# Optimization experiments

Measured on AMD Instinct MI355X. Metric: run time of the kernel, lower is better.

The kernel has to match this reference:

```python
import jax, jax.numpy as jnp
import numpy as np

C = 1.0          # ball curvature (k = -1/c with c=1.0 in the torch module)
SQC = 1.0        # sqrt(C)
LN_EPS = 1e-5

def _artanh(x):
    return jnp.arctanh(jnp.clip(x, -1.0 + 1e-7, 1.0 - 1e-7))

def _norm(x):
    # last-dim L2 norm, clamped away from zero for stable division
    return jnp.clip(jnp.sqrt(jnp.sum(x * x, axis=-1, keepdims=True)), 1e-7, None)

def expmap0(u):
    un = _norm(u)
    return jnp.tanh(SQC * un) * u / (SQC * un)

def logmap0(y):
    yn = _norm(y)
    return _artanh(SQC * yn) * y / (SQC * yn)

def mobius_add(x, y):
    x2 = jnp.sum(x * x, axis=-1, keepdims=True)
    y2 = jnp.sum(y * y, axis=-1, keepdims=True)
    xy = jnp.sum(x * y, axis=-1, keepdims=True)
    num = (1.0 + 2.0 * C * xy + C * y2) * x + (1.0 - C * x2) * y
    den = 1.0 + 2.0 * C * xy + C * C * x2 * y2
    return num / jnp.clip(den, 1e-15, None)

def mobius_matvec(W, x):
    # W: [H, D], x: [B, D] -> [B, H]
    mx = x @ W.T
    xn = _norm(x)
    mxn = _norm(mx)
    res = jnp.tanh(mxn / xn * _artanh(SQC * xn)) * mx / (SQC * mxn)
    return jnp.where(mxn <= 1e-7, jnp.zeros_like(res), res)

def mobius_pointwise_mul(w, x):
    wx = w * x
    xn = _norm(x)
    wxn = _norm(wx)
    res = jnp.tanh(wxn / xn * _artanh(SQC * xn)) * wx / (SQC * wxn)
    return jnp.where(wxn <= 1e-7, jnp.zeros_like(res), res)

def layer_norm(x, g, b):
    mu = jnp.mean(x, axis=-1, keepdims=True)
    var = jnp.mean((x - mu) ** 2, axis=-1, keepdims=True)
    return (x - mu) * jax.lax.rsqrt(var + LN_EPS) * g + b

def one_rnn_transform(W, h, U, x, b):
    Wh = mobius_matvec(W, h)
    Ux = mobius_matvec(U, x)
    return mobius_add(mobius_add(Wh, Ux), b)

def setup_inputs() -> dict:
    key = jax.random.key(0)
    B, I, H = 65536, 256, 256
    k1, k2, k3, k4, k5 = jax.random.split(key, 5)
    stdv = 1.0 / np.sqrt(H)
    # points on the Poincare ball via expmap0 of small tangent vectors
    x = expmap0(0.02 * jax.random.normal(k1, (B, I), dtype=jnp.float32))
    hx = expmap0(0.02 * jax.random.normal(k2, (B, H), dtype=jnp.float32))
    weight_ih = jax.random.uniform(k3, (3 * H, I), dtype=jnp.float32, minval=-stdv, maxval=stdv)
    weight_hh = jax.random.uniform(k4, (3 * H, H), dtype=jnp.float32, minval=-stdv, maxval=stdv)
    bias = 0.01 * jax.random.normal(k5, (3, H), dtype=jnp.float32)
    ln_gamma = jnp.ones((3, H), dtype=jnp.float32)
    ln_beta = jnp.zeros((3, H), dtype=jnp.float32)
    return {"input": x, "hx": hx, "weight_ih": weight_ih, "weight_hh": weight_hh,
            "bias": bias, "ln_gamma": ln_gamma, "ln_beta": ln_beta}

def reference(input, hx, weight_ih, weight_hh, bias, ln_gamma, ln_beta):
    H = hx.shape[-1]
    W_ir, W_ih_, W_iz = weight_ih[:H], weight_ih[H:2*H], weight_ih[2*H:]
    W_hr, W_hh_, W_hz = weight_hh[:H], weight_hh[H:2*H], weight_hh[2*H:]
    b_r, b_h, b_z = bias[0], bias[1], bias[2]
    temp_z = logmap0(one_rnn_transform(W_hz, hx, W_iz, input, b_z))
    temp_r = logmap0(one_rnn_transform(W_hr, hx, W_ir, input, b_r))
    z_t = jax.nn.sigmoid(layer_norm(temp_z, ln_gamma[0], ln_beta[0]))
    r_t = jax.nn.sigmoid(layer_norm(temp_r, ln_gamma[1], ln_beta[1]))
    rh_t = mobius_pointwise_mul(r_t, hx)
    h_tilde = one_rnn_transform(W_hh_, rh_t, W_ih_, input, b_h)
    h_tilde = expmap0(jnp.tanh(layer_norm(logmap0(h_tilde), ln_gamma[2], ln_beta[2])))
    temp_1 = mobius_pointwise_mul(1.0 - z_t, hx)
    temp_2 = mobius_pointwise_mul(z_t, h_tilde)
    return mobius_add(temp_1, temp_2)
```

## Files before the change

kernel.cpp:

```cpp
#include <hip/hip_runtime.h>
#include <math.h>

#define HD  256
#define BM  16
#define NTH 256

typedef __attribute__((ext_vector_type(8))) short bf16x8;
typedef __attribute__((ext_vector_type(4))) float f32x4;

__device__ __forceinline__ float rcp_f(float x){ return __builtin_amdgcn_rcpf(x); }
__device__ __forceinline__ float tanh_f(float x){
  float ax = fabsf(x);
  float e  = __expf(-2.f*ax);
  float t  = (1.f - e) * rcp_f(1.f + e);
  return copysignf(t, x);
}
__device__ __forceinline__ float artanh_f(float v){
  v = fminf(fmaxf(v, -1.f + 1e-7f), 1.f - 1e-7f);
  return 0.5f * __logf((1.f + v) * rcp_f(1.f - v));
}
__device__ __forceinline__ float sigmoid_f(float v){ return rcp_f(1.f + __expf(-v)); }
__device__ __forceinline__ unsigned short f2bf(float f){
  unsigned u = __float_as_uint(f);
  u += 0x7FFFu + ((u >> 16) & 1u);
  return (unsigned short)(u >> 16);
}
__device__ __forceinline__ float bf2f(unsigned short h){
  return __uint_as_float(((unsigned)h) << 16);
}
__device__ __forceinline__ int swz(int R, int C){
  return R*HD + (((C >> 3) ^ (R & 7)) << 3) + (C & 7);
}

__global__ void convert_w_kernel(const float* __restrict__ Wih,
                                 const float* __restrict__ Whh,
                                 unsigned short* __restrict__ wb){
  int c = blockIdx.x * blockDim.x + threadIdx.x;
  if (c >= 6 * 8192) return;
  int mat = c >> 13;
  int ci  = c & 8191;
  int l = ci & 63, st = ci >> 6;
  int s = st & 7, ct = st >> 3;
  int col = ct * 16 + (l & 15);
  int k0  = s * 32 + (l >> 4) * 8;
  const float* src = (mat < 3) ? (Wih + (size_t)mat * HD * HD)
                               : (Whh + (size_t)(mat - 3) * HD * HD);
  const float* p = src + (size_t)col * HD + k0;
  unsigned short tmp[8];
  #pragma unroll
  for (int j = 0; j < 8; ++j) tmp[j] = f2bf(p[j]);
  *(bf16x8*)(wb + (size_t)mat * 65536 + (size_t)ci * 8) = *(bf16x8*)tmp;
}

__device__ __forceinline__ void gate_gemm(
    const unsigned short* ldsH, const unsigned short* __restrict__ wH,
    const unsigned short* ldsX, const unsigned short* __restrict__ wX,
    f32x4 A[4], f32x4 Bx[4], int wc, int lr, int lg, int l){
  #pragma unroll
  for (int n = 0; n < 4; ++n){
    A[n]  = (f32x4){0.f,0.f,0.f,0.f};
    Bx[n] = (f32x4){0.f,0.f,0.f,0.f};
  }
  #pragma unroll
  for (int s = 0; s < 8; ++s){
    int idx = lr*HD + (((4*s + lg) ^ (lr & 7)) << 3);
    bf16x8 ah = *(const bf16x8*)&ldsH[idx];
    bf16x8 ax = *(const bf16x8*)&ldsX[idx];
    #pragma unroll
    for (int n = 0; n < 4; ++n){
      int ct = wc*4 + n;
      int off = ((ct*8 + s)*64 + l)*8;
      bf16x8 bh = *(const bf16x8*)(wH + off);
      bf16x8 bx = *(const bf16x8*)(wX + off);
      A[n]  = __builtin_amdgcn_mfma_f32_16x16x32_bf16(ah, bh, A[n], 0, 0, 0);
      Bx[n] = __builtin_amdgcn_mfma_f32_16x16x32_bf16(ax, bx, Bx[n], 0, 0, 0);
    }
  }
}

__device__ __forceinline__ void gate_reduce_chain(
    const f32x4 (&A)[4], const f32x4 (&Bx)[4], const float (&bt)[4],
    float (*RED)[33], float (*kco)[9], float (*srow)[BM], const float* sbb,
    int rowA, int gidx, int t, int wc, int lr, int lg){
  float p[7][4];
  #pragma unroll
  for (int q = 0; q < 4; ++q){
    float a2=0.f,b2=0.f,ab=0.f,sA=0.f,sB=0.f,Ab=0.f,Bb=0.f;
    #pragma unroll
    for (int n = 0; n < 4; ++n){
      float ae = A[n][q], be = Bx[n][q], bv = bt[n];
      a2 = fmaf(ae,ae,a2); b2 = fmaf(be,be,b2); ab = fmaf(ae,be,ab);
      sA += ae; sB += be; Ab = fmaf(ae,bv,Ab); Bb = fmaf(be,bv,Bb);
    }
    p[0][q]=a2; p[1][q]=b2; p[2][q]=ab; p[3][q]=sA; p[4][q]=sB; p[5][q]=Ab; p[6][q]=Bb;
  }
  #pragma unroll
  for (int j = 0; j < 7; ++j)
    #pragma unroll
    for (int q = 0; q < 4; ++q){
      float v = p[j][q];
      v += __shfl_xor(v,1); v += __shfl_xor(v,2);
      v += __shfl_xor(v,4); v += __shfl_xor(v,8);
      p[j][q] = v;
    }
  if (lr == 0){
    #pragma unroll
    for (int q = 0; q < 4; ++q){
      int R = lg*4 + q;
      #pragma unroll
      for (int j = 0; j < 7; ++j) RED[R][wc*8 + j] = p[j][q];
    }
  }
  __syncthreads();
  if (t < BM){
    int R = t;
    float s[7];
    #pragma unroll
    for (int j = 0; j < 7; ++j)
      s[j] = RED[R][j] + RED[R][8+j] + RED[R][16+j] + RED[R][24+j];
    float bb  = sbb[gidx];
    float sbs = sbb[4+gidx];
    float an = srow[rowA][R], aa = srow[rowA+1][R];
    float bn = srow[0][R],    ba = srow[1][R];
    float mraw = sqrtf(s[0]); float mA = fmaxf(mraw, 1e-7f);
    float tA = tanh_f(mA / an * aa);
    float sa  = (mraw <= 1e-7f) ? 0.f : tA / mA;
    float x2a = (mraw <= 1e-7f) ? 0.f : tA*tA;
    float nraw = sqrtf(s[1]); float mB = fmaxf(nraw, 1e-7f);
    float tB = tanh_f(mB / bn * ba);
    float sb_ = (nraw <= 1e-7f) ? 0.f : tB / mB;
    float x2b = (nraw <= 1e-7f) ? 0.f : tB*tB;
    float xy = sa*sb_*s[2];
    float ca = 1.f + 2.f*xy + x2b;
    float cb = 1.f - x2a;
    float den = fmaxf(1.f + 2.f*xy + x2a*x2b, 1e-15f);
    float u = ca*sa/den, v = cb*sb_/den;
    float P2 = u*u*s[0] + 2.f*u*v*s[2] + v*v*s[1];
    float Pb = u*s[5] + v*s[6];
    float sP = u*s[3] + v*s[4];
    float ca2 = 1.f + 2.f*Pb + bb;
    float cb2 = 1.f - P2;
    float den2 = fmaxf(1.f + 2.f*Pb + P2*bb, 1e-15f);
    float pp = ca2/den2, ww = cb2/den2;
    float Q2 = pp*pp*P2 + 2.f*pp*ww*Pb + ww*ww*bb;
    float sQsum = pp*sP + ww*sbs;
    float qn = fmaxf(sqrtf(Q2), 1e-7f);
    float sQ = artanh_f(qn) / qn;
    float mu = sQ*sQsum*(1.f/HD);
    float e2 = sQ*sQ*Q2*(1.f/HD);
    float is = rsqrtf(e2 - mu*mu + 1e-5f);
    kco[R][0] = sQ*pp*u;  kco[R][1] = sQ*pp*v;  kco[R][2] = sQ*ww;
    kco[R][3] = mu;       kco[R][4] = is;
  }
  __syncthreads();
}

__global__ __launch_bounds__(NTH, 2) void mobius_gru_mfma(
    const float* __restrict__ x, const float* __restrict__ hx,
    const unsigned short* __restrict__ wbih, const unsigned short* __restrict__ wbhh,
    const float* __restrict__ bias, const float* __restrict__ gam,
    const float* __restrict__ bet, float* __restrict__ out, int B){
  __shared__ unsigned short xb[BM*HD];
  __shared__ unsigned short hb[BM*HD];
  __shared__ float RED[BM][33];
  __shared__ float kco[BM][9];
  __shared__ float srow[8][BM];
  __shared__ float sbb[8];

  const int t  = threadIdx.x;
  const int l  = t & 63;
  const int lr = l & 15, lg = l >> 4;
  const int wc = t >> 6;
  const size_t row0 = (size_t)blockIdx.x * BM;

  {
    float* spart = &RED[0][0];
    int r = t >> 4, seg = t & 15;
    const float* xp = x  + (row0 + r)*HD + seg*16;
    const float* hp = hx + (row0 + r)*HD + seg*16;
    float sx = 0.f, sh = 0.f;
    #pragma unroll
    for (int i = 0; i < 4; ++i){
      int c = seg*16 + i*4;
      int di = swz(r, c);
      float4 v = *(const float4*)(xp + i*4);
      sx += v.x*v.x + v.y*v.y + v.z*v.z + v.w*v.w;
      ushort4 o = { f2bf(v.x), f2bf(v.y), f2bf(v.z), f2bf(v.w) };
      *(ushort4*)&xb[di] = o;
      v = *(const float4*)(hp + i*4);
      sh += v.x*v.x + v.y*v.y + v.z*v.z + v.w*v.w;
      ushort4 o2 = { f2bf(v.x), f2bf(v.y), f2bf(v.z), f2bf(v.w) };
      *(ushort4*)&hb[di] = o2;
    }
    spart[r*16 + seg] = sx; spart[256 + r*16 + seg] = sh;
  }
  if (t >= 64 && t < 256){
    int g = (t >> 6) - 1;
    float4 b4 = *(const float4*)&bias[g*HD + (t & 63)*4];
    float p2 = b4.x*b4.x + b4.y*b4.y + b4.z*b4.z + b4.w*b4.w;
    float ps = b4.x + b4.y + b4.z + b4.w;
    #pragma unroll
    for (int m = 1; m <= 32; m <<= 1){ p2 += __shfl_xor(p2, m); ps += __shfl_xor(ps, m); }
    if ((t & 63) == 0){ sbb[g] = p2; sbb[4+g] = ps; }
  }
  __syncthreads();
  if (t < BM){
    float* spart = &RED[0][0];
    float sx = 0.f, sh = 0.f;
    #pragma unroll
    for (int i = 0; i < 16; ++i){ sx += spart[t*16 + i]; sh += spart[256 + t*16 + i]; }
    float xn = fmaxf(sqrtf(sx), 1e-7f);
    float hn = fmaxf(sqrtf(sh), 1e-7f);
    srow[0][t] = xn; srow[1][t] = artanh_f(xn);
    srow[2][t] = hn; srow[3][t] = artanh_f(hn);
  }
  __syncthreads();

  f32x4 A[4], Bx[4];
  float bt[4], gv[4], bv[4];
  unsigned ztp[4][2];
  float hvreg[4][4];

  #pragma unroll
  for (int n = 0; n < 4; ++n){
    int C = wc*64 + n*16 + lr;
    bt[n] = bias[2*HD + C]; gv[n] = gam[C]; bv[n] = bet[C];
  }
  gate_gemm(hb, wbhh + 2*65536, xb, wbih + 2*65536, A, Bx, wc, lr, lg, l);
  gate_reduce_chain(A, Bx, bt, RED, kco, srow, sbb, 2, 2, t, wc, lr, lg);
  #pragma unroll
  for (int q = 0; q < 4; ++q){
    int R = lg*4 + q;
    float KA=kco[R][0], KB=kco[R][1], Kb=kco[R][2], mu=kco[R][3], is=kco[R][4];
    #pragma unroll
    for (int n = 0; n < 4; ++n){
      float ln = (KA*A[n][q] + KB*Bx[n][q] + Kb*bt[n] - mu)*is*gv[n] + bv[n];
      unsigned zb = f2bf(sigmoid_f(ln));
      if ((q & 1) == 0) ztp[n][q>>1] = zb;
      else              ztp[n][q>>1] |= (zb << 16);
    }
  }

  #pragma unroll
  for (int n = 0; n < 4; ++n){
    int C = wc*64 + n*16 + lr;
    bt[n] = bias[C]; gv[n] = gam[HD + C]; bv[n] = bet[HD + C];
  }
  gate_gemm(hb, wbhh, xb, wbih, A, Bx, wc, lr, lg, l);
  gate_reduce_chain(A, Bx, bt, RED, kco, srow, sbb, 2, 0, t, wc, lr, lg);
  {
    #pragma unroll
    for (int q = 0; q < 4; ++q){
      int R = lg*4 + q;
      float KA=kco[R][0], KB=kco[R][1], Kb=kco[R][2], mu=kco[R][3], is=kco[R][4];
      float acc = 0.f;
      #pragma unroll
      for (int n = 0; n < 4; ++n){
        int C = wc*64 + n*16 + lr;
        float hv = bf2f(hb[swz(R, C)]);
        hvreg[n][q] = hv;
        float ln = (KA*A[n][q] + KB*Bx[n][q] + Kb*bt[n] - mu)*is*gv[n] + bv[n];
        float rhv = sigmoid_f(ln) * hv;
        Bx[n][q] = rhv;
        acc = fmaf(rhv, rhv, acc);
      }
      float v2 = acc;
      v2 += __shfl_xor(v2,1); v2 += __shfl_xor(v2,2);
      v2 += __shfl_xor(v2,4); v2 += __shfl_xor(v2,8);
      if (lr == 0) RED[R][wc*8] = v2;
    }
  }
  __syncthreads();
  if (t < BM){
    int R = t;
    float s0 = RED[R][0] + RED[R][8] + RED[R][16] + RED[R][24];
    float wraw = sqrtf(s0); float wn = fmaxf(wraw, 1e-7f);
    float s = tanh_f(wn / srow[2][R] * srow[3][R]);
    float sc = (wraw <= 1e-7f) ? 0.f : s / wn;
    float rn = fmaxf((wraw <= 1e-7f) ? 0.f : fabsf(s), 1e-7f);
    kco[R][0] = sc; srow[4][R] = rn; srow[5][R] = artanh_f(rn);
  }
  __syncthreads();
  #pragma unroll
  for (int q = 0; q < 4; ++q){
    int R = lg*4 + q;
    float sc = kco[R][0];
    #pragma unroll
    for (int n = 0; n < 4; ++n){
      int C = wc*64 + n*16 + lr;
      hb[swz(R, C)] = f2bf(sc * Bx[n][q]);
    }
  }
  __syncthreads();

  #pragma unroll
  for (int n = 0; n < 4; ++n){
    int C = wc*64 + n*16 + lr;
    bt[n] = bias[HD + C]; gv[n] = gam[2*HD + C]; bv[n] = bet[2*HD + C];
  }
  gate_gemm(hb, wbhh + 65536, xb, wbih + 65536, A, Bx, wc, lr, lg, l);
  gate_reduce_chain(A, Bx, bt, RED, kco, srow, sbb, 4, 1, t, wc, lr, lg);
  {
    #pragma unroll
    for (int q = 0; q < 4; ++q){
      int R = lg*4 + q;
      float KA=kco[R][0], KB=kco[R][1], Kb=kco[R][2], mu=kco[R][3], is=kco[R][4];
      float acc = 0.f;
      #pragma unroll
      for (int n = 0; n < 4; ++n){
        float ln = (KA*A[n][q] + KB*Bx[n][q] + Kb*bt[n] - mu)*is*gv[n] + bv[n];
        float uv = tanh_f(ln);
        A[n][q] = uv;
        acc = fmaf(uv, uv, acc);
      }
      float v2 = acc;
      v2 += __shfl_xor(v2,1); v2 += __shfl_xor(v2,2);
      v2 += __shfl_xor(v2,4); v2 += __shfl_xor(v2,8);
      if (lr == 0) RED[R][wc*8] = v2;
    }
  }
  __syncthreads();
  if (t < BM){
    int R = t;
    float s0 = RED[R][0] + RED[R][8] + RED[R][16] + RED[R][24];
    float unraw = sqrtf(s0);
    float un = fmaxf(unraw, 1e-7f);
    float es = tanh_f(un) / un;
    float htn = fmaxf(es * unraw, 1e-7f);
    kco[R][0] = es; srow[6][R] = htn; srow[7][R] = artanh_f(htn);
  }
  __syncthreads();

  #pragma unroll
  for (int q = 0; q < 4; ++q){
    int R = lg*4 + q;
    float es = kco[R][0];
    float a1 = 0.f, a2 = 0.f, a12 = 0.f;
    #pragma unroll
    for (int n = 0; n < 4; ++n){
      unsigned zp = ztp[n][q >> 1];
      float zv = __uint_as_float((q & 1) ? (zp & 0xFFFF0000u) : (zp << 16));
      float w2v = zv * es * A[n][q];
      float w1v = (1.f - zv) * hvreg[n][q];
      A[n][q]  = w1v;
      Bx[n][q] = w2v;
      a1 = fmaf(w1v, w1v, a1); a2 = fmaf(w2v, w2v, a2); a12 = fmaf(w1v, w2v, a12);
    }
    float v1 = a1, v2 = a2, v3 = a12;
    v1 += __shfl_xor(v1,1); v2 += __shfl_xor(v2,1); v3 += __shfl_xor(v3,1);
    v1 += __shfl_xor(v1,2); v2 += __shfl_xor(v2,2); v3 += __shfl_xor(v3,2);
    v1 += __shfl_xor(v1,4); v2 += __shfl_xor(v2,4); v3 += __shfl_xor(v3,4);
    v1 += __shfl_xor(v1,8); v2 += __shfl_xor(v2,8); v3 += __shfl_xor(v3,8);
    if (lr == 0){
      RED[R][wc*8]   = v1;
      RED[R][wc*8+1] = v2;
      RED[R][wc*8+2] = v3;
    }
  }
  __syncthreads();
  if (t < BM){
    int R = t;
    float s1  = RED[R][0] + RED[R][8]  + RED[R][16] + RED[R][24];
    float s2  = RED[R][1] + RED[R][9]  + RED[R][17] + RED[R][25];
    float s12 = RED[R][2] + RED[R][10] + RED[R][18] + RED[R][26];
    float raw1 = sqrtf(s1); float n1 = fmaxf(raw1, 1e-7f);
    float ss1 = tanh_f(n1 / srow[2][R] * srow[3][R]);
    float sc1 = (raw1 <= 1e-7f) ? 0.f : ss1 / n1;
    float t1  = (raw1 <= 1e-7f) ? 0.f : ss1*ss1;
    float raw2 = sqrtf(s2); float n2 = fmaxf(raw2, 1e-7f);
    float ss2 = tanh_f(n2 / srow[6][R] * srow[7][R]);
    float sc2 = (raw2 <= 1e-7f) ? 0.f : ss2 / n2;
    float t2  = (raw2 <= 1e-7f) ? 0.f : ss2*ss2;
    float xy = sc1*sc2*s12;
    float ca = 1.f + 2.f*xy + t2;
    float cb = 1.f - t1;
    float den = fmaxf(1.f + 2.f*xy + t1*t2, 1e-15f);
    kco[R][0] = ca*sc1/den;
    kco[R][1] = cb*sc2/den;
  }
  __syncthreads();
  #pragma unroll
  for (int q = 0; q < 4; ++q){
    int R = lg*4 + q;
    float cw1 = kco[R][0], cw2 = kco[R][1];
    #pragma unroll
    for (int n = 0; n < 4; ++n){
      int C = wc*64 + n*16 + lr;
      out[(row0 + R)*HD + C] = cw1*A[n][q] + cw2*Bx[n][q];
    }
  }
}

extern "C" void kernel_launch(void* const* d_in, const int* in_sizes, int n_in,
                              void* d_out, int out_size, void* d_ws, size_t ws_size,
                              hipStream_t stream){
  const float* x    = (const float*)d_in[0];
  const float* hx   = (const float*)d_in[1];
  const float* Wih  = (const float*)d_in[2];
  const float* Whh  = (const float*)d_in[3];
  const float* bias = (const float*)d_in[4];
  const float* gam  = (const float*)d_in[5];
  const float* bet  = (const float*)d_in[6];
  float* out = (float*)d_out;
  unsigned short* wb = (unsigned short*)d_ws;
  const int B = in_sizes[0] / HD;

  hipLaunchKernelGGL(convert_w_kernel, dim3(192), dim3(256), 0, stream, Wih, Whh, wb);
  hipLaunchKernelGGL(mobius_gru_mfma, dim3(B / BM), dim3(NTH), 0, stream,
                     x, hx, wb, wb + 3*65536, bias, gam, bet, out, B);
}
```

Before: 222.8 us.

## Fuse z, r and x-side h-gate GEMMs into one pass with shared reductions

Merges the z-gate and r-gate GEMMs, plus the input-side GEMM of the candidate gate, into a single k-loop that reuses the LDS A-fragments for five MFMA streams. The z and r per-row reduction chains now run together in 32 threads with separate reduction buffers, which removes several barrier rounds. Register pressure rises a lot (five accumulator sets of 4 f32x4 each live at once), which could cause spills or lower occupancy under the 2-block launch bound.

```diff
diff --git a/kernel.cpp b/kernel.cpp
--- a/kernel.cpp
+++ b/kernel.cpp
@@ -52,43 +52,16 @@
   *(bf16x8*)(wb + (size_t)mat * 65536 + (size_t)ci * 8) = *(bf16x8*)tmp;
 }
 
-__device__ __forceinline__ void gate_gemm(
-    const unsigned short* ldsH, const unsigned short* __restrict__ wH,
-    const unsigned short* ldsX, const unsigned short* __restrict__ wX,
-    f32x4 A[4], f32x4 Bx[4], int wc, int lr, int lg, int l){
-  #pragma unroll
-  for (int n = 0; n < 4; ++n){
-    A[n]  = (f32x4){0.f,0.f,0.f,0.f};
-    Bx[n] = (f32x4){0.f,0.f,0.f,0.f};
-  }
-  #pragma unroll
-  for (int s = 0; s < 8; ++s){
-    int idx = lr*HD + (((4*s + lg) ^ (lr & 7)) << 3);
-    bf16x8 ah = *(const bf16x8*)&ldsH[idx];
-    bf16x8 ax = *(const bf16x8*)&ldsX[idx];
-    #pragma unroll
-    for (int n = 0; n < 4; ++n){
-      int ct = wc*4 + n;
-      int off = ((ct*8 + s)*64 + l)*8;
-      bf16x8 bh = *(const bf16x8*)(wH + off);
-      bf16x8 bx = *(const bf16x8*)(wX + off);
-      A[n]  = __builtin_amdgcn_mfma_f32_16x16x32_bf16(ah, bh, A[n], 0, 0, 0);
-      Bx[n] = __builtin_amdgcn_mfma_f32_16x16x32_bf16(ax, bx, Bx[n], 0, 0, 0);
-    }
-  }
-}
-
-__device__ __forceinline__ void gate_reduce_chain(
-    const f32x4 (&A)[4], const f32x4 (&Bx)[4], const float (&bt)[4],
-    float (*RED)[33], float (*kco)[9], float (*srow)[BM], const float* sbb,
-    int rowA, int gidx, int t, int wc, int lr, int lg){
+__device__ __forceinline__ void reduce7(
+    const f32x4* A, const f32x4* B, const float* bt,
+    float (*RED)[33], int wc, int lr, int lg){
   float p[7][4];
   #pragma unroll
   for (int q = 0; q < 4; ++q){
     float a2=0.f,b2=0.f,ab=0.f,sA=0.f,sB=0.f,Ab=0.f,Bb=0.f;
     #pragma unroll
     for (int n = 0; n < 4; ++n){
-      float ae = A[n][q], be = Bx[n][q], bv = bt[n];
+      float ae = A[n][q], be = B[n][q], bv = bt[n];
       a2 = fmaf(ae,ae,a2); b2 = fmaf(be,be,b2); ab = fmaf(ae,be,ab);
       sA += ae; sB += be; Ab = fmaf(ae,bv,Ab); Bb = fmaf(be,bv,Bb);
     }
@@ -111,48 +84,40 @@
       for (int j = 0; j < 7; ++j) RED[R][wc*8 + j] = p[j][q];
     }
   }
-  __syncthreads();
-  if (t < BM){
-    int R = t;
-    float s[7];
-    #pragma unroll
-    for (int j = 0; j < 7; ++j)
-      s[j] = RED[R][j] + RED[R][8+j] + RED[R][16+j] + RED[R][24+j];
-    float bb  = sbb[gidx];
-    float sbs = sbb[4+gidx];
-    float an = srow[rowA][R], aa = srow[rowA+1][R];
-    float bn = srow[0][R],    ba = srow[1][R];
-    float mraw = sqrtf(s[0]); float mA = fmaxf(mraw, 1e-7f);
-    float tA = tanh_f(mA / an * aa);
-    float sa  = (mraw <= 1e-7f) ? 0.f : tA / mA;
-    float x2a = (mraw <= 1e-7f) ? 0.f : tA*tA;
-    float nraw = sqrtf(s[1]); float mB = fmaxf(nraw, 1e-7f);
-    float tB = tanh_f(mB / bn * ba);
-    float sb_ = (nraw <= 1e-7f) ? 0.f : tB / mB;
-    float x2b = (nraw <= 1e-7f) ? 0.f : tB*tB;
-    float xy = sa*sb_*s[2];
-    float ca = 1.f + 2.f*xy + x2b;
-    float cb = 1.f - x2a;
-    float den = fmaxf(1.f + 2.f*xy + x2a*x2b, 1e-15f);
-    float u = ca*sa/den, v = cb*sb_/den;
-    float P2 = u*u*s[0] + 2.f*u*v*s[2] + v*v*s[1];
-    float Pb = u*s[5] + v*s[6];
-    float sP = u*s[3] + v*s[4];
-    float ca2 = 1.f + 2.f*Pb + bb;
-    float cb2 = 1.f - P2;
-    float den2 = fmaxf(1.f + 2.f*Pb + P2*bb, 1e-15f);
-    float pp = ca2/den2, ww = cb2/den2;
-    float Q2 = pp*pp*P2 + 2.f*pp*ww*Pb + ww*ww*bb;
-    float sQsum = pp*sP + ww*sbs;
-    float qn = fmaxf(sqrtf(Q2), 1e-7f);
-    float sQ = artanh_f(qn) / qn;
-    float mu = sQ*sQsum*(1.f/HD);
-    float e2 = sQ*sQ*Q2*(1.f/HD);
-    float is = rsqrtf(e2 - mu*mu + 1e-5f);
-    kco[R][0] = sQ*pp*u;  kco[R][1] = sQ*pp*v;  kco[R][2] = sQ*ww;
-    kco[R][3] = mu;       kco[R][4] = is;
-  }
-  __syncthreads();
+}
+
+__device__ __forceinline__ void chain5(
+    const float* s, float bb, float sbs,
+    float an, float aa, float bn, float ba, float* o){
+  float mraw = sqrtf(s[0]); float mA = fmaxf(mraw, 1e-7f);
+  float tA = tanh_f(mA / an * aa);
+  float sa  = (mraw <= 1e-7f) ? 0.f : tA / mA;
+  float x2a = (mraw <= 1e-7f) ? 0.f : tA*tA;
+  float nraw = sqrtf(s[1]); float mB = fmaxf(nraw, 1e-7f);
+  float tB = tanh_f(mB / bn * ba);
+  float sb_ = (nraw <= 1e-7f) ? 0.f : tB / mB;
+  float x2b = (nraw <= 1e-7f) ? 0.f : tB*tB;
+  float xy = sa*sb_*s[2];
+  float ca = 1.f + 2.f*xy + x2b;
+  float cb = 1.f - x2a;
+  float den = fmaxf(1.f + 2.f*xy + x2a*x2b, 1e-15f);
+  float u = ca*sa/den, v = cb*sb_/den;
+  float P2 = u*u*s[0] + 2.f*u*v*s[2] + v*v*s[1];
+  float Pb = u*s[5] + v*s[6];
+  float sP = u*s[3] + v*s[4];
+  float ca2 = 1.f + 2.f*Pb + bb;
+  float cb2 = 1.f - P2;
+  float den2 = fmaxf(1.f + 2.f*Pb + P2*bb, 1e-15f);
+  float pp = ca2/den2, ww = cb2/den2;
+  float Q2 = pp*pp*P2 + 2.f*pp*ww*Pb + ww*ww*bb;
+  float sQsum = pp*sP + ww*sbs;
+  float qn = fmaxf(sqrtf(Q2), 1e-7f);
+  float sQ = artanh_f(qn) / qn;
+  float mu = sQ*sQsum*(1.f/HD);
+  float e2 = sQ*sQ*Q2*(1.f/HD);
+  float is = rsqrtf(e2 - mu*mu + 1e-5f);
+  o[0] = sQ*pp*u;  o[1] = sQ*pp*v;  o[2] = sQ*ww;
+  o[3] = mu;       o[4] = is;
 }
 
 __global__ __launch_bounds__(NTH, 2) void mobius_gru_mfma(
@@ -162,8 +127,9 @@
     const float* __restrict__ bet, float* __restrict__ out, int B){
   __shared__ unsigned short xb[BM*HD];
   __shared__ unsigned short hb[BM*HD];
-  __shared__ float RED[BM][33];
-  __shared__ float kco[BM][9];
+  __shared__ float REDZ[BM][33];
+  __shared__ float REDR[BM][33];
+  __shared__ float kco[BM][10];
   __shared__ float srow[8][BM];
   __shared__ float sbb[8];
 
@@ -174,7 +140,7 @@
   const size_t row0 = (size_t)blockIdx.x * BM;
 
   {
-    float* spart = &RED[0][0];
+    float* spart = &REDZ[0][0];
     int r = t >> 4, seg = t & 15;
     const float* xp = x  + (row0 + r)*HD + seg*16;
     const float* hp = hx + (row0 + r)*HD + seg*16;
@@ -205,7 +171,7 @@
   }
   __syncthreads();
   if (t < BM){
-    float* spart = &RED[0][0];
+    float* spart = &REDZ[0][0];
     float sx = 0.f, sh = 0.f;
     #pragma unroll
     for (int i = 0; i < 16; ++i){ sx += spart[t*16 + i]; sh += spart[256 + t*16 + i]; }
@@ -216,39 +182,166 @@
   }
   __syncthreads();
 
-  f32x4 A[4], Bx[4];
-  float bt[4], gv[4], bv[4];
+  f32x4 Az[4], Bz[4], Ar[4], Br[4], Bh[4];
+  float btz[4], btr[4];
+  #pragma unroll
+  for (int n = 0; n < 4; ++n){
+    int C = wc*64 + n*16 + lr;
+    btz[n] = bias[2*HD + C];
+    btr[n] = bias[C];
+    Az[n] = (f32x4){0.f,0.f,0.f,0.f}; Bz[n] = (f32x4){0.f,0.f,0.f,0.f};
+    Ar[n] = (f32x4){0.f,0.f,0.f,0.f}; Br[n] = (f32x4){0.f,0.f,0.f,0.f};
+    Bh[n] = (f32x4){0.f,0.f,0.f,0.f};
+  }
+  {
+    const unsigned short* wHz = wbhh + 2*65536;
+    const unsigned short* wXz = wbih + 2*65536;
+    const unsigned short* wHr = wbhh;
+    const unsigned short* wXr = wbih;
+    const unsigned short* wXh = wbih + 65536;
+    #pragma unroll
+    for (int s = 0; s < 8; ++s){
+      int idx = lr*HD + (((4*s + lg) ^ (lr & 7)) << 3);
+      bf16x8 ah = *(const bf16x8*)&hb[idx];
+      bf16x8 ax = *(const bf16x8*)&xb[idx];
+      #pragma unroll
+      for (int n = 0; n < 4; ++n){
+        int off = (((wc*4 + n)*8 + s)*64 + l)*8;
+        bf16x8 bhz = *(const bf16x8*)(wHz + off);
+        bf16x8 bxz = *(const bf16x8*)(wXz + off);
+        bf16x8 bhr = *(const bf16x8*)(wHr + off);
+        bf16x8 bxr = *(const bf16x8*)(wXr + off);
+        bf16x8 bxh = *(const bf16x8*)(wXh + off);
+        Az[n] = __builtin_amdgcn_mfma_f32_16x16x32_bf16(ah, bhz, Az[n], 0, 0, 0);
+        Bz[n] = __builtin_amdgcn_mfma_f32_16x16x32_bf16(ax, bxz, Bz[n], 0, 0, 0);
+        Ar[n] = __builtin_amdgcn_mfma_f32_16x16x32_bf16(ah, bhr, Ar[n], 0, 0, 0);
+        Br[n] = __builtin_amdgcn_mfma_f32_16x16x32_bf16(ax, bxr, Br[n], 0, 0, 0);
+        Bh[n] = __builtin_amdgcn_mfma_f32_16x16x32_bf16(ax, bxh, Bh[n], 0, 0, 0);
+      }
+    }
+  }
+  reduce7(Az, Bz, btz, REDZ, wc, lr, lg);
+  reduce7(Ar, Br, btr, REDR, wc, lr, lg);
+  __syncthreads();
+  if (t < 32){
+    int R = t & 15, gsel = t >> 4;
+    float (*REDp)[33] = gsel ? REDR : REDZ;
+    int gidx = gsel ? 0 : 2;
+    float s[7];
+    #pragma unroll
+    for (int j = 0; j < 7; ++j)
+      s[j] = REDp[R][j] + REDp[R][8+j] + REDp[R][16+j] + REDp[R][24+j];
+    float o[5];
+    chain5(s, sbb[gidx], sbb[4+gidx],
+           srow[2][R], srow[3][R], srow[0][R], srow[1][R], o);
+    #pragma unroll
+    for (int k = 0; k < 5; ++k) kco[R][gsel*5 + k] = o[k];
+  }
+  __syncthreads();
+
   unsigned ztp[4][2];
   float hvreg[4][4];
-
+  {
+    float gvz[4], bvz[4], gvr[4], bvr[4];
+    #pragma unroll
+    for (int n = 0; n < 4; ++n){
+      int C = wc*64 + n*16 + lr;
+      gvz[n] = gam[C];      bvz[n] = bet[C];
+      gvr[n] = gam[HD + C]; bvr[n] = bet[HD + C];
+    }
+    #pragma unroll
+    for (int q = 0; q < 4; ++q){
+      int R = lg*4 + q;
+      float KAz=kco[R][0], KBz=kco[R][1], Kbz=kco[R][2], muz=kco[R][3], isz=kco[R][4];
+      float KAr=kco[R][5], KBr=kco[R][6], Kbr=kco[R][7], mur=kco[R][8], isr=kco[R][9];
+      float acc = 0.f;
+      #pragma unroll
+      for (int n = 0; n < 4; ++n){
+        int C = wc*64 + n*16 + lr;
+        float hv = bf2f(hb[swz(R, C)]);
+        hvreg[n][q] = hv;
+        float lnz = (KAz*Az[n][q] + KBz*Bz[n][q] + Kbz*btz[n] - muz)*isz*gvz[n] + bvz[n];
+        unsigned zb = f2bf(sigmoid_f(lnz));
+        if ((q & 1) == 0) ztp[n][q>>1] = zb;
+        else              ztp[n][q>>1] |= (zb << 16);
+        float lnr = (KAr*Ar[n][q] + KBr*Br[n][q] + Kbr*btr[n] - mur)*isr*gvr[n] + bvr[n];
+        float rhv = sigmoid_f(lnr) * hv;
+        Br[n][q] = rhv;
+        acc = fmaf(rhv, rhv, acc);
+      }
+      float v2 = acc;
+      v2 += __shfl_xor(v2,1); v2 += __shfl_xor(v2,2);
+      v2 += __shfl_xor(v2,4); v2 += __shfl_xor(v2,8);
+      if (lr == 0) REDZ[R][wc*8] = v2;
+    }
+  }
+  __syncthreads();
+  if (t < BM){
+    int R = t;
+    float s0 = REDZ[R][0] + REDZ[R][8] + REDZ[R][16] + REDZ[R][24];
+    float wraw = sqrtf(s0); float wn = fmaxf(wraw, 1e-7f);
+    float s = tanh_f(wn / srow[2][R] * srow[3][R]);
+    float sc = (wraw <= 1e-7f) ? 0.f : s / wn;
+    float rn = fmaxf((wraw <= 1e-7f) ? 0.f : fabsf(s), 1e-7f);
+    kco[R][0] = sc; srow[4][R] = rn; srow[5][R] = artanh_f(rn);
+  }
+  __syncthreads();
+  #pragma unroll
+  for (int q = 0; q < 4; ++q){
+    int R = lg*4 + q;
+    float sc = kco[R][0];
+    #pragma unroll
+    for (int n = 0; n < 4; ++n){
+      int C = wc*64 + n*16 + lr;
+      hb[swz(R, C)] = f2bf(sc * Br[n][q]);
+    }
+  }
+  __syncthreads();
+
+  f32x4 Ah[4];
+  float bth[4];
   #pragma unroll
   for (int n = 0; n < 4; ++n){
     int C = wc*64 + n*16 + lr;
-    bt[n] = bias[2*HD + C]; gv[n] = gam[C]; bv[n] = bet[C];
-  }
-  gate_gemm(hb, wbhh + 2*65536, xb, wbih + 2*65536, A, Bx, wc, lr, lg, l);
-  gate_reduce_chain(A, Bx, bt, RED, kco, srow, sbb, 2, 2, t, wc, lr, lg);
-  #pragma unroll
-  for (int q = 0; q < 4; ++q){
-    int R = lg*4 + q;
-    float KA=kco[R][0], KB=kco[R][1], Kb=kco[R][2], mu=kco[R][3], is=kco[R][4];
-    #pragma unroll
-    for (int n = 0; n < 4; ++n){
-      float ln = (KA*A[n][q] + KB*Bx[n][q] + Kb*bt[n] - mu)*is*gv[n] + bv[n];
-      unsigned zb = f2bf(sigmoid_f(ln));
-      if ((q & 1) == 0) ztp[n][q>>1] = zb;
-      else              ztp[n][q>>1] |= (zb << 16);
-    }
-  }
-
-  #pragma unroll
-  for (int n = 0; n < 4; ++n){
-    int C = wc*64 + n*16 + lr;
-    bt[n] = bias[C]; gv[n] = gam[HD + C]; bv[n] = bet[HD + C];
-  }
-  gate_gemm(hb, wbhh, xb, wbih, A, Bx, wc, lr, lg, l);
-  gate_reduce_chain(A, Bx, bt, RED, kco, srow, sbb, 2, 0, t, wc, lr, lg);
+    bth[n] = bias[HD + C];
+    Ah[n] = (f32x4){0.f,0.f,0.f,0.f};
+  }
   {
+    const unsigned short* wHh = wbhh + 65536;
+    #pragma unroll
+    for (int s = 0; s < 8; ++s){
+      int idx = lr*HD + (((4*s + lg) ^ (lr & 7)) << 3);
+      bf16x8 ar = *(const bf16x8*)&hb[idx];
+      #pragma unroll
+      for (int n = 0; n < 4; ++n){
+        int off = (((wc*4 + n)*8 + s)*64 + l)*8;
+        bf16x8 bh = *(const bf16x8*)(wHh + off);
+        Ah[n] = __builtin_amdgcn_mfma_f32_16x16x32_bf16(ar, bh, Ah[n], 0, 0, 0);
+      }
+    }
+  }
+  reduce7(Ah, Bh, bth, REDZ, wc, lr, lg);
+  __syncthreads();
+  if (t < BM){
+    int R = t;
+    float s[7];
+    #pragma unroll
+    for (int j = 0; j < 7; ++j)
+      s[j] = REDZ[R][j] + REDZ[R][8+j] + REDZ[R][16+j] + REDZ[R][24+j];
+    float o[5];
+    chain5(s, sbb[1], sbb[5],
+           srow[4][R], srow[5][R], srow[0][R], srow[1][R], o);
+    #pragma unroll
+    for (int k = 0; k < 5; ++k) kco[R][k] = o[k];
+  }
+  __syncthreads();
+  {
+    float gvh[4], bvh[4];
+    #pragma unroll
+    for (int n = 0; n < 4; ++n){
+      int C = wc*64 + n*16 + lr;
+      gvh[n] = gam[2*HD + C]; bvh[n] = bet[2*HD + C];
+    }
     #pragma unroll
     for (int q = 0; q < 4; ++q){
       int R = lg*4 + q;
@@ -256,73 +349,21 @@
       float acc = 0.f;
       #pragma unroll
       for (int n = 0; n < 4; ++n){
-        int C = wc*64 + n*16 + lr;
-        float hv = bf2f(hb[swz(R, C)]);
-        hvreg[n][q] = hv;
-        float ln = (KA*A[n][q] + KB*Bx[n][q] + Kb*bt[n] - mu)*is*gv[n] + bv[n];
-        float rhv = sigmoid_f(ln) * hv;
-        Bx[n][q] = rhv;
-        acc = fmaf(rhv, rhv, acc);
-      }
-      float v2 = acc;
-      v2 += __shfl_xor(v2,1); v2 += __shfl_xor(v2,2);
-      v2 += __shfl_xor(v2,4); v2 += __shfl_xor(v2,8);
-      if (lr == 0) RED[R][wc*8] = v2;
-    }
-  }
-  __syncthreads();
-  if (t < BM){
-    int R = t;
-    float s0 = RED[R][0] + RED[R][8] + RED[R][16] + RED[R][24];
-    float wraw = sqrtf(s0); float wn = fmaxf(wraw, 1e-7f);
-    float s = tanh_f(wn / srow[2][R] * srow[3][R]);
-    float sc = (wraw <= 1e-7f) ? 0.f : s / wn;
-    float rn = fmaxf((wraw <= 1e-7f) ? 0.f : fabsf(s), 1e-7f);
-    kco[R][0] = sc; srow[4][R] = rn; srow[5][R] = artanh_f(rn);
-  }
-  __syncthreads();
-  #pragma unroll
-  for (int q = 0; q < 4; ++q){
-    int R = lg*4 + q;
-    float sc = kco[R][0];
-    #pragma unroll
-    for (int n = 0; n < 4; ++n){
-      int C = wc*64 + n*16 + lr;
-      hb[swz(R, C)] = f2bf(sc * Bx[n][q]);
-    }
-  }
-  __syncthreads();
-
-  #pragma unroll
-  for (int n = 0; n < 4; ++n){
-    int C = wc*64 + n*16 + lr;
-    bt[n] = bias[HD + C]; gv[n] = gam[2*HD + C]; bv[n] = bet[2*HD + C];
-  }
-  gate_gemm(hb, wbhh + 65536, xb, wbih + 65536, A, Bx, wc, lr, lg, l);
-  gate_reduce_chain(A, Bx, bt, RED, kco, srow, sbb, 4, 1, t, wc, lr, lg);
-  {
-    #pragma unroll
-    for (int q = 0; q < 4; ++q){
-      int R = lg*4 + q;
-      float KA=kco[R][0], KB=kco[R][1], Kb=kco[R][2], mu=kco[R][3], is=kco[R][4];
-      float acc = 0.f;
-      #pragma unroll
-      for (int n = 0; n < 4; ++n){
-        float ln = (KA*A[n][q] + KB*Bx[n][q] + Kb*bt[n] - mu)*is*gv[n] + bv[n];
+        float ln = (KA*Ah[n][q] + KB*Bh[n][q] + Kb*bth[n] - mu)*is*gvh[n] + bvh[n];
         float uv = tanh_f(ln);
-        A[n][q] = uv;
+        Ah[n][q] = uv;
         acc = fmaf(uv, uv, acc);
       }
       float v2 = acc;
       v2 += __shfl_xor(v2,1); v2 += __shfl_xor(v2,2);
       v2 += __shfl_xor(v2,4); v2 += __shfl_xor(v2,8);
-      if (lr == 0) RED[R][wc*8] = v2;
+      if (lr == 0) REDZ[R][wc*8] = v2;
     }
   }
   __syncthreads();
   if (t < BM){
     int R = t;
-    float s0 = RED[R][0] + RED[R][8] + RED[R][16] + RED[R][24];
+    float s0 = REDZ[R][0] + REDZ[R][8] + REDZ[R][16] + REDZ[R][24];
     float unraw = sqrtf(s0);
     float un = fmaxf(unraw, 1e-7f);
     float es = tanh_f(un) / un;
@@ -340,10 +381,10 @@
     for (int n = 0; n < 4; ++n){
       unsigned zp = ztp[n][q >> 1];
       float zv = __uint_as_float((q & 1) ? (zp & 0xFFFF0000u) : (zp << 16));
-      float w2v = zv * es * A[n][q];
+      float w2v = zv * es * Ah[n][q];
       float w1v = (1.f - zv) * hvreg[n][q];
-      A[n][q]  = w1v;
-      Bx[n][q] = w2v;
+      Ah[n][q] = w2v;
+      Bh[n][q] = w1v;
       a1 = fmaf(w1v, w1v, a1); a2 = fmaf(w2v, w2v, a2); a12 = fmaf(w1v, w2v, a12);
     }
     float v1 = a1, v2 = a2, v3 = a12;
@@ -352,17 +393,17 @@
     v1 += __shfl_xor(v1,4); v2 += __shfl_xor(v2,4); v3 += __shfl_xor(v3,4);
     v1 += __shfl_xor(v1,8); v2 += __shfl_xor(v2,8); v3 += __shfl_xor(v3,8);
     if (lr == 0){
-      RED[R][wc*8]   = v1;
-      RED[R][wc*8+1] = v2;
-      RED[R][wc*8+2] = v3;
+      REDZ[R][wc*8]   = v1;
+      REDZ[R][wc*8+1] = v2;
+      REDZ[R][wc*8+2] = v3;
     }
   }
   __syncthreads();
   if (t < BM){
     int R = t;
-    float s1  = RED[R][0] + RED[R][8]  + RED[R][16] + RED[R][24];
-    float s2  = RED[R][1] + RED[R][9]  + RED[R][17] + RED[R][25];
-    float s12 = RED[R][2] + RED[R][10] + RED[R][18] + RED[R][26];
+    float s1  = REDZ[R][0] + REDZ[R][8]  + REDZ[R][16] + REDZ[R][24];
+    float s2  = REDZ[R][1] + REDZ[R][9]  + REDZ[R][17] + REDZ[R][25];
+    float s12 = REDZ[R][2] + REDZ[R][10] + REDZ[R][18] + REDZ[R][26];
     float raw1 = sqrtf(s1); float n1 = fmaxf(raw1, 1e-7f);
     float ss1 = tanh_f(n1 / srow[2][R] * srow[3][R]);
     float sc1 = (raw1 <= 1e-7f) ? 0.f : ss1 / n1;
@@ -386,7 +427,7 @@
     #pragma unroll
     for (int n = 0; n < 4; ++n){
       int C = wc*64 + n*16 + lr;
-      out[(row0 + R)*HD + C] = cw1*A[n][q] + cw2*Bx[n][q];
+      out[(row0 + R)*HD + C] = cw1*Bh[n][q] + cw2*Ah[n][q];
     }
   }
 }
```

Result: no change. 219.1 us (-1.7%).
